# Kernel tuning notes

Measured on AMD Instinct MI355X. Metric: run time of the kernel, lower is better.

Reference implementation:

```python
import jax, jax.numpy as jnp
import numpy as np

M, K, N = 8192, 4096, 4096

def setup_inputs() -> dict:
    key = jax.random.key(0)
    k1, k2, k3, k4 = jax.random.split(key, 4)
    x = jax.random.normal(k1, (M, K), dtype=jnp.float32)
    # pre-quantized int8 weights [K, N] and per-output-channel scales [N]
    weight_q = jax.random.randint(k2, (K, N), -128, 128, dtype=jnp.int32).astype(jnp.int8)
    weight_scale = (jax.random.uniform(k3, (N,), dtype=jnp.float32) * 0.01 + 1e-4)
    bias = jax.random.normal(k4, (N,), dtype=jnp.float32) * 0.02
    return {"x": x, "weight_q": weight_q, "weight_scale": weight_scale, "bias": bias}

def reference(x, weight_q, weight_scale, bias):
    # dynamic per-row int8 quantization of activations
    max_vals = jnp.max(jnp.abs(x), axis=-1, keepdims=True)          # [M, 1]
    a_scale = jnp.maximum(max_vals / 127.0, 1e-8)                    # [M, 1]
    x_q = jnp.clip(jnp.round(x / a_scale), -128, 127).astype(jnp.int8)
    c = jnp.matmul(x_q.astype(jnp.float32), weight_q.astype(jnp.float32))  # [M, N]
    # dequantize: per-row activation scale * per-column weight scale
    c = c * a_scale * weight_scale[None, :]
    out = c.astype(x.dtype) + bias
    return out
```

## Files before the change

kernel.cpp:

```cpp
#include <hip/hip_runtime.h>


typedef int   int32x4  __attribute__((ext_vector_type(4)));
typedef int   int32x16 __attribute__((ext_vector_type(16)));
typedef float floatx4  __attribute__((ext_vector_type(4)));

#define BM 128
#define BN 128
#define BK 128

__device__ __forceinline__ void async_copy16(const void* g, void* l) {
    __builtin_amdgcn_global_load_lds(
        (const __attribute__((address_space(1))) unsigned int*)g,
        (__attribute__((address_space(3))) unsigned int*)l,
        16, 0, 0);
}

__device__ __forceinline__ int quant1(float x, float s) {
    float q = rintf(x / s);
    q = fminf(127.0f, fmaxf(-128.0f, q));
    return (int)q;
}

__global__ __launch_bounds__(256) void prep_kernel(
    const float* __restrict__ x, const int* __restrict__ Bq,
    signed char* __restrict__ xq, signed char* __restrict__ Bt,
    float* __restrict__ ascale, int M, int K, int N)
{
    __shared__ __align__(16) int shmem[64 * 17];
    const int t = threadIdx.x;
    const int b = (int)blockIdx.x;

    if (b < M) {
        const int row = b;
        const float4* xr4 = (const float4*)(x + (size_t)row * K);
        float4 v[4];
        float mx = 0.0f;
#pragma unroll
        for (int i = 0; i < 4; ++i) {
            v[i] = xr4[t * 4 + i];
            mx = fmaxf(mx, fmaxf(fmaxf(fabsf(v[i].x), fabsf(v[i].y)),
                                 fmaxf(fabsf(v[i].z), fabsf(v[i].w))));
        }
#pragma unroll
        for (int off = 32; off > 0; off >>= 1)
            mx = fmaxf(mx, __shfl_xor(mx, off, 64));
        float* wmax = (float*)shmem;
        if ((t & 63) == 0) wmax[t >> 6] = mx;
        __syncthreads();
        mx = fmaxf(fmaxf(wmax[0], wmax[1]), fmaxf(wmax[2], wmax[3]));

        const float s = fmaxf(mx / 127.0f, 1e-8f);
        if (t == 0) ascale[row] = s;

        int out[4];
#pragma unroll
        for (int i = 0; i < 4; ++i) {
            const int b0 = quant1(v[i].x, s);
            const int b1 = quant1(v[i].y, s);
            const int b2 = quant1(v[i].z, s);
            const int b3 = quant1(v[i].w, s);
            out[i] = (b0 & 255) | ((b1 & 255) << 8) | ((b2 & 255) << 16) | ((b3 & 255) << 24);
        }
        *(int32x4*)(xq + (size_t)row * K + t * 16) = *(const int32x4*)out;
    } else {
        const int tile = b - M;
        const int tiles_n = N >> 6;
        const int n0 = (tile % tiles_n) * 64;
        const int k0 = (tile / tiles_n) * 64;

        const int r = t >> 4;
        const int ncol = (t & 15) * 4;

        const int* src = Bq + (size_t)(k0 + 4 * r) * N + n0 + ncol;
        const int4 u0 = *(const int4*)(src);
        const int4 u1 = *(const int4*)(src + N);
        const int4 u2 = *(const int4*)(src + 2 * (size_t)N);
        const int4 u3 = *(const int4*)(src + 3 * (size_t)N);

        shmem[(ncol + 0) * 17 + r] = (u0.x & 255) | ((u1.x & 255) << 8) | ((u2.x & 255) << 16) | ((u3.x & 255) << 24);
        shmem[(ncol + 1) * 17 + r] = (u0.y & 255) | ((u1.y & 255) << 8) | ((u2.y & 255) << 16) | ((u3.y & 255) << 24);
        shmem[(ncol + 2) * 17 + r] = (u0.z & 255) | ((u1.z & 255) << 8) | ((u2.z & 255) << 16) | ((u3.z & 255) << 24);
        shmem[(ncol + 3) * 17 + r] = (u0.w & 255) | ((u1.w & 255) << 8) | ((u2.w & 255) << 16) | ((u3.w & 255) << 24);
        __syncthreads();

        const int nl = t >> 2, ch = t & 3;
        int o[4];
#pragma unroll
        for (int i = 0; i < 4; ++i) o[i] = shmem[nl * 17 + ch * 4 + i];
        *(int32x4*)(Bt + (size_t)(n0 + nl) * K + k0 + ch * 16) = *(const int32x4*)o;
    }
}

__global__ __launch_bounds__(256, 3) void gemm_i8_kernel(
    const signed char* __restrict__ Aq, const signed char* __restrict__ Bt,
    const float* __restrict__ ascale, const float* __restrict__ wscale,
    const float* __restrict__ bias, float* __restrict__ C,
    int M, int N, int K)
{
    __shared__ __align__(16) signed char As[BM * BK];
    __shared__ __align__(16) signed char Bs[BN * BK];

    const int t = threadIdx.x;
    const int lane = t & 63;
    const int w = t >> 6;
    const int wr = w >> 1, wc = w & 1;

    const int m0 = blockIdx.y * BM;
    const int n0 = blockIdx.x * BN;

    const int srow = t >> 3;
    const int schunk = ((t & 7) ^ (srow & 7)) * 16;
    const signed char* gA = Aq + (size_t)(m0 + srow) * K + schunk;
    const signed char* gB = Bt + (size_t)(n0 + srow) * K + schunk;
    signed char* lA = As + t * 16;
    signed char* lB = Bs + t * 16;

    const int ml = lane & 31;
    const int half = lane >> 5;
    const int sw = ml & 7;
    const signed char* fA0 = As + (wr * 64 + ml) * BK;
    const signed char* fA1 = fA0 + 32 * BK;
    const signed char* fB0 = Bs + (wc * 64 + ml) * BK;
    const signed char* fB1 = fB0 + 32 * BK;

    int32x16 acc[2][2] = {};

    for (int k0 = 0; k0 < K; k0 += BK) {
#pragma unroll
        for (int r = 0; r < 8; ++r)
            async_copy16(gA + k0 + (size_t)r * 32 * K, lA + r * 4096);
#pragma unroll
        for (int r = 0; r < 8; ++r)
            async_copy16(gB + k0 + (size_t)r * 32 * K, lB + r * 4096);
        __syncthreads();

#pragma unroll
        for (int kk = 0; kk < 4; ++kk) {
            const int chunk = kk * 2 + half;
            const int off = ((chunk ^ sw) * 16);
            int32x4 a0 = *(const int32x4*)(fA0 + off);
            int32x4 a1 = *(const int32x4*)(fA1 + off);
            int32x4 b0 = *(const int32x4*)(fB0 + off);
            int32x4 b1 = *(const int32x4*)(fB1 + off);
            acc[0][0] = __builtin_amdgcn_mfma_i32_32x32x32_i8(a0, b0, acc[0][0], 0, 0, 0);
            acc[0][1] = __builtin_amdgcn_mfma_i32_32x32x32_i8(a0, b1, acc[0][1], 0, 0, 0);
            acc[1][0] = __builtin_amdgcn_mfma_i32_32x32x32_i8(a1, b0, acc[1][0], 0, 0, 0);
            acc[1][1] = __builtin_amdgcn_mfma_i32_32x32x32_i8(a1, b1, acc[1][1], 0, 0, 0);
        }
        __syncthreads();
    }

    const int rowoff = 4 * half;
#pragma unroll
    for (int j = 0; j < 2; ++j) {
        const int col = n0 + wc * 64 + j * 32 + ml;
        const float ws = wscale[col];
        const float bs = bias[col];
#pragma unroll
        for (int i = 0; i < 2; ++i) {
            const int rbase = m0 + wr * 64 + i * 32 + rowoff;
#pragma unroll
            for (int g = 0; g < 4; ++g) {
                const int rg = rbase + 8 * g;
                const floatx4 as4 = *(const floatx4*)(ascale + rg);
                float* cp = C + (size_t)rg * N + col;
#pragma unroll
                for (int rr = 0; rr < 4; ++rr) {
                    cp[(size_t)rr * N] = ((float)acc[i][j][g * 4 + rr] * as4[rr]) * ws + bs;
                }
            }
        }
    }
}

extern "C" void kernel_launch(void* const* d_in, const int* in_sizes, int n_in,
                              void* d_out, int out_size, void* d_ws, size_t ws_size,
                              hipStream_t stream) {
    const float* x      = (const float*)d_in[0];
    const int*   wq     = (const int*)d_in[1];
    const float* wscale = (const float*)d_in[2];
    const float* bias   = (const float*)d_in[3];
    float* out          = (float*)d_out;

    const int N = in_sizes[2];
    const int K = in_sizes[1] / N;
    const int M = in_sizes[0] / K;

    char* ws = (char*)d_ws;
    signed char* xq = (signed char*)ws;
    signed char* bt = (signed char*)(ws + (size_t)M * K);
    float* ascale   = (float*)(ws + (size_t)M * K + (size_t)N * K);

    const int prep_blocks = M + (N / 64) * (K / 64);
    prep_kernel<<<prep_blocks, 256, 0, stream>>>(x, wq, xq, bt, ascale, M, K, N);
    gemm_i8_kernel<<<dim3(N / BN, M / BM), 256, 0, stream>>>(
        xq, bt, ascale, wscale, bias, out, M, N, K);
}
```

Before: 443.9 us.

## Halve GEMM K-tile to 64, adjust swizzle, and coalesce prep row loads

The GEMM K-tile shrinks from 128 to 64, which halves LDS use per block (16 KB instead of 32 KB) and cuts the async copies per thread from 16 to 4 per iteration. The XOR swizzle and fragment offsets are changed to match the 4-chunk row. The launch-bounds occupancy hint drops from 3 to 2 blocks per CU. The prep kernel now reads and writes activation rows with a stride of 256 elements between each thread's iterations, so a wavefront's accesses are contiguous. The smaller K-tile doubles the number of barrier round-trips, and there is still no double buffering to overlap loads with MFMA work.

```diff
diff --git a/kernel.cpp b/kernel.cpp
--- a/kernel.cpp
+++ b/kernel.cpp
@@ -7,7 +7,7 @@
 
 #define BM 128
 #define BN 128
-#define BK 128
+#define BK 64
 
 __device__ __forceinline__ void async_copy16(const void* g, void* l) {
     __builtin_amdgcn_global_load_lds(
@@ -38,7 +38,7 @@
         float mx = 0.0f;
 #pragma unroll
         for (int i = 0; i < 4; ++i) {
-            v[i] = xr4[t * 4 + i];
+            v[i] = xr4[i * 256 + t];
             mx = fmaxf(mx, fmaxf(fmaxf(fabsf(v[i].x), fabsf(v[i].y)),
                                  fmaxf(fabsf(v[i].z), fabsf(v[i].w))));
         }
@@ -53,16 +53,16 @@
         const float s = fmaxf(mx / 127.0f, 1e-8f);
         if (t == 0) ascale[row] = s;
 
-        int out[4];
+        int* xqi = (int*)(xq + (size_t)row * K);
 #pragma unroll
         for (int i = 0; i < 4; ++i) {
             const int b0 = quant1(v[i].x, s);
             const int b1 = quant1(v[i].y, s);
             const int b2 = quant1(v[i].z, s);
             const int b3 = quant1(v[i].w, s);
-            out[i] = (b0 & 255) | ((b1 & 255) << 8) | ((b2 & 255) << 16) | ((b3 & 255) << 24);
-        }
-        *(int32x4*)(xq + (size_t)row * K + t * 16) = *(const int32x4*)out;
+            xqi[i * 256 + t] =
+                (b0 & 255) | ((b1 & 255) << 8) | ((b2 & 255) << 16) | ((b3 & 255) << 24);
+        }
     } else {
         const int tile = b - M;
         const int tiles_n = N >> 6;
@@ -92,7 +92,7 @@
     }
 }
 
-__global__ __launch_bounds__(256, 3) void gemm_i8_kernel(
+__global__ __launch_bounds__(256, 2) void gemm_i8_kernel(
     const signed char* __restrict__ Aq, const signed char* __restrict__ Bt,
     const float* __restrict__ ascale, const float* __restrict__ wscale,
     const float* __restrict__ bias, float* __restrict__ C,
@@ -109,16 +109,20 @@
     const int m0 = blockIdx.y * BM;
     const int n0 = blockIdx.x * BN;
 
-    const int srow = t >> 3;
-    const int schunk = ((t & 7) ^ (srow & 7)) * 16;
-    const signed char* gA = Aq + (size_t)(m0 + srow) * K + schunk;
-    const signed char* gB = Bt + (size_t)(n0 + srow) * K + schunk;
-    signed char* lA = As + t * 16;
-    signed char* lB = Bs + t * 16;
+    const int srow = t >> 2;
+    const int schunk = ((t & 3) ^ (srow & 3)) * 16;
+    const signed char* gA0 = Aq + (size_t)(m0 + srow) * K + schunk;
+    const signed char* gA1 = gA0 + (size_t)64 * K;
+    const signed char* gB0 = Bt + (size_t)(n0 + srow) * K + schunk;
+    const signed char* gB1 = gB0 + (size_t)64 * K;
+    signed char* lA0 = As + t * 16;
+    signed char* lA1 = lA0 + 4096;
+    signed char* lB0 = Bs + t * 16;
+    signed char* lB1 = lB0 + 4096;
 
     const int ml = lane & 31;
     const int half = lane >> 5;
-    const int sw = ml & 7;
+    const int sw = ml & 3;
     const signed char* fA0 = As + (wr * 64 + ml) * BK;
     const signed char* fA1 = fA0 + 32 * BK;
     const signed char* fB0 = Bs + (wc * 64 + ml) * BK;
@@ -127,18 +131,15 @@
     int32x16 acc[2][2] = {};
 
     for (int k0 = 0; k0 < K; k0 += BK) {
-#pragma unroll
-        for (int r = 0; r < 8; ++r)
-            async_copy16(gA + k0 + (size_t)r * 32 * K, lA + r * 4096);
-#pragma unroll
-        for (int r = 0; r < 8; ++r)
-            async_copy16(gB + k0 + (size_t)r * 32 * K, lB + r * 4096);
-        __syncthreads();
-
-#pragma unroll
-        for (int kk = 0; kk < 4; ++kk) {
-            const int chunk = kk * 2 + half;
-            const int off = ((chunk ^ sw) * 16);
+        async_copy16(gA0 + k0, lA0);
+        async_copy16(gA1 + k0, lA1);
+        async_copy16(gB0 + k0, lB0);
+        async_copy16(gB1 + k0, lB1);
+        __syncthreads();
+
+#pragma unroll
+        for (int kk = 0; kk < 2; ++kk) {
+            const int off = (((kk * 2 + half) ^ sw) * 16);
             int32x4 a0 = *(const int32x4*)(fA0 + off);
             int32x4 a1 = *(const int32x4*)(fA1 + off);
             int32x4 b0 = *(const int32x4*)(fB0 + off);
```

After: 438.5 us. About the same (-1.2%).
